# Performance work log

Measured on AMD Instinct MI355X. Metric: run time of the kernel, lower is better.

## Reference

```python
import jax, jax.numpy as jnp
import numpy as np

T = 4096   # total packed tokens
NQ = 16    # query heads
NK = 4     # kv heads (GQA)
HN = 128   # head dim


def setup_inputs() -> dict:
    key = jax.random.key(0)
    kq, kk, kv = jax.random.split(key, 3)
    return {
        "query": jax.random.normal(kq, (T, NQ, HN), dtype=jnp.float32),
        "key": jax.random.normal(kk, (T, NK, HN), dtype=jnp.float32),
        "value": jax.random.normal(kv, (T, NK, HN), dtype=jnp.float32),
        # packed varlen boundaries (4 sequences)
        "cu_seqlens": jnp.array([0, 1536, 2048, 3584, 4096], dtype=jnp.int32),
    }


def reference(query, key, value, cu_seqlens):
    t, nq, hn = query.shape
    nk = key.shape[1]
    rep = nq // nk  # GQA expansion factor
    scale = hn ** -0.5
    # [h, t, d] layout (matches torch unsqueeze(0).permute(0,2,1,3), batch=1)
    q = jnp.transpose(query, (1, 0, 2))
    k = jnp.repeat(jnp.transpose(key, (1, 0, 2)), rep, axis=0)
    v = jnp.repeat(jnp.transpose(value, (1, 0, 2)), rep, axis=0)
    # full scores [h, t, t]
    scores = jnp.einsum('hqd,hkd->hqk', q, k) * scale
    # block-diagonal causal mask from cu_seqlens
    idx = jnp.arange(t)
    seg = jnp.searchsorted(cu_seqlens[1:], idx, side='right')  # segment id per token
    allowed = (seg[:, None] == seg[None, :]) & (idx[None, :] <= idx[:, None])
    scores = jnp.where(allowed[None, :, :], scores, -jnp.inf)
    p = jax.nn.softmax(scores, axis=-1)  # every row keeps its diagonal -> no NaN
    out = jnp.einsum('hqk,hkd->hqd', p, v)
    # [t, nq*hn]
    return jnp.transpose(out, (1, 0, 2)).reshape(t, nq * hn)
```

## Files before the change

### kernel.cpp

```cpp
#include <hip/hip_runtime.h>
#include <hip/hip_bf16.h>
#include <cstdint>
#include <cstddef>

#define NQH 16
#define NKH 4
#define HN 128
#define QBLK 64
#define KBLK 32
#define QSCALE 0.12751589542585458f

typedef __bf16 bf16x8 __attribute__((ext_vector_type(8)));
typedef float f32x4 __attribute__((ext_vector_type(4)));

__device__ __forceinline__ void gload16(const void* g, void* l) {
  __builtin_amdgcn_global_load_lds(
      (const __attribute__((address_space(1))) void*)g,
      (__attribute__((address_space(3))) void*)l, 16, 0, 0);
}

__global__ __launch_bounds__(256) void cvt_kv(const float* __restrict__ K,
                                              const float* __restrict__ V,
                                              __bf16* __restrict__ Kb,
                                              __bf16* __restrict__ Vb, int T) {
  const int nkblk = T * NKH * HN / 8 / 256;
  const int bid = blockIdx.x;
  if (bid < nkblk) {
    const size_t idx8 = ((size_t)bid * 256 + threadIdx.x) * 8;
    const int d = (int)(idx8 & 127);
    const int kvh = (int)((idx8 >> 7) & 3);
    const size_t t = idx8 >> 9;
    float4 a = *(const float4*)&K[idx8];
    float4 b = *(const float4*)&K[idx8 + 4];
    bf16x8 f;
    f[0] = (__bf16)a.x; f[1] = (__bf16)a.y; f[2] = (__bf16)a.z; f[3] = (__bf16)a.w;
    f[4] = (__bf16)b.x; f[5] = (__bf16)b.y; f[6] = (__bf16)b.z; f[7] = (__bf16)b.w;
    *(bf16x8*)&Kb[(size_t)kvh * T * HN + t * HN + d] = f;
  } else {
    const int ob = (bid - nkblk) * 2 + (threadIdx.x >> 7);
    const int bx = ob & (T / 8 - 1);
    const int kvh = ob / (T / 8);
    const int d = threadIdx.x & 127;
    const int t0 = bx * 8;
    bf16x8 f;
#pragma unroll
    for (int i = 0; i < 8; ++i)
      f[i] = (__bf16)V[(size_t)(t0 + i) * (NKH * HN) + kvh * HN + d];
    *(bf16x8*)&Vb[(size_t)kvh * HN * T + (size_t)d * T + t0] = f;
  }
}

template <bool MASKED>
__device__ __forceinline__ void attn_iter(
    const char* Kc, const char* Vc, const bf16x8 qfA[4], const bf16x8 qfB[4],
    int ln, int hi, int vslot, int limA, float& lA, f32x4* accA,
    float& lB, f32x4* accB) {
  bf16x8 kf[2][4];
#pragma unroll
  for (int c = 0; c < 2; ++c)
#pragma unroll
    for (int kc = 0; kc < 4; ++kc)
      kf[c][kc] = *(const bf16x8*)(Kc + (c * 16 + ln) * 256 +
                                   (((kc * 4 + hi) ^ (ln & 7)) << 4));

  f32x4 sA[2], sB[2];
#pragma unroll
  for (int c = 0; c < 2; ++c) {
    sA[c] = (f32x4){0.f, 0.f, 0.f, 0.f};
    sB[c] = (f32x4){0.f, 0.f, 0.f, 0.f};
  }
  __builtin_amdgcn_s_setprio(1);
#pragma unroll
  for (int kc = 0; kc < 4; ++kc) {
#pragma unroll
    for (int c = 0; c < 2; ++c) {
      sA[c] = __builtin_amdgcn_mfma_f32_16x16x32_bf16(kf[c][kc], qfA[kc], sA[c], 0, 0, 0);
      sB[c] = __builtin_amdgcn_mfma_f32_16x16x32_bf16(kf[c][kc], qfB[kc], sB[c], 0, 0, 0);
    }
  }
  __builtin_amdgcn_s_setprio(0);

  if (MASKED) {
    const int limB = limA + 16;
#pragma unroll
    for (int c = 0; c < 2; ++c)
#pragma unroll
      for (int i = 0; i < 4; ++i) {
        const int koff = hi * 8 + c * 4 + i;
        sA[c][i] = (koff <= limA) ? sA[c][i] : -1e30f;
        sB[c][i] = (koff <= limB) ? sB[c][i] : -1e30f;
      }
  }

  float pA[2][4], pB[2][4];
  float psA = 0.f, psB = 0.f;
#pragma unroll
  for (int c = 0; c < 2; ++c)
#pragma unroll
    for (int i = 0; i < 4; ++i) {
      pA[c][i] = exp2f(sA[c][i]); psA += pA[c][i];
      pB[c][i] = exp2f(sB[c][i]); psB += pB[c][i];
    }
  lA += psA; lB += psB;

  bf16x8 paA, paB;
#pragma unroll
  for (int e = 0; e < 8; ++e) {
    paA[e] = (__bf16)pA[e >> 2][e & 3];
    paB[e] = (__bf16)pB[e >> 2][e & 3];
  }

  __builtin_amdgcn_s_setprio(1);
#pragma unroll
  for (int dt = 0; dt < 8; ++dt) {
    const bf16x8 vb = *(const bf16x8*)(Vc + (dt * 16 + ln) * 64 + vslot);
    accA[dt] = __builtin_amdgcn_mfma_f32_16x16x32_bf16(vb, paA, accA[dt], 0, 0, 0);
    accB[dt] = __builtin_amdgcn_mfma_f32_16x16x32_bf16(vb, paB, accB[dt], 0, 0, 0);
  }
  __builtin_amdgcn_s_setprio(0);
}

__global__ __launch_bounds__(256, 2) void attn_jobs(
    const float* __restrict__ Q, const __bf16* __restrict__ Kb,
    const __bf16* __restrict__ Vb, const int* __restrict__ cu,
    float* __restrict__ O, int T, int nseg) {
  const int tid = threadIdx.x;
  const int w = tid >> 6, lane = tid & 63;
  const int g = w >> 1, wv = w & 1;
  const int ln = lane & 15, hi = lane >> 4;
  const int b = blockIdx.x;

  __shared__ __align__(16) char smem[66304];
  float* l1s = (float*)(smem + 65536);
  int* s_r2t = (int*)(smem + 65792);

  if (w == 0) {
    const int t2 = lane;
    const int r0t = t2 << 6;
    int st = 0;
    for (int s = 1; s < nseg; ++s) { const int c = cu[s]; if (c <= r0t) st = c; }
    const int dep = r0t + QBLK - st;
    int rk = 0;
    for (int j = 0; j < 64; ++j) {
      const int dj = __shfl(dep, j);
      rk += (dj > dep) || (dj == dep && j < t2);
    }
    s_r2t[rk] = t2;
  }
  __syncthreads();

  const int gl = wv * 64 + lane;
  const int Rb = gl >> 4, sK = gl & 15;
  int key_j[4];
#pragma unroll
  for (int j = 0; j < 4; ++j)
    key_j[j] = ((Rb >> 2) << 3) + (Rb & 3) + ((j & 1) << 4) + ((j >> 1) << 2);
  const int kcolE = (sK ^ Rb) << 3;
  const int d = gl >> 2, sV = gl & 3;
  const int swz_d = (d & 3) ^ ((d >> 2) & 3);
  const int vkeyE = (sV ^ swz_d) << 3;
  const int vslot = ((hi ^ (ln & 3) ^ ((ln >> 2) & 3)) << 4);
  const int relA = wv * 32 + ln;

#pragma unroll 1
  for (int job = 0; job < 2; ++job) {
    if (job) __syncthreads();
    const int rank = job ? (1023 - b) : b;
    const int h = rank & 15;
    const int kvh = h >> 2;
    const int r0 = s_r2t[rank >> 4] << 6;

    int st0 = 0;
    for (int s = 1; s < nseg; ++s) { const int c = cu[s]; if (c <= r0) st0 = c; }
    const int kstart = st0;
    const int n0 = (r0 + QBLK - kstart) >> 6;
    const int gbeg = kstart + g * n0 * KBLK;

    const __bf16* KbH = Kb + (size_t)kvh * T * HN;
    const __bf16* VbH = Vb + (size_t)kvh * HN * T;

    bf16x8 qfA[4], qfB[4];
    {
      const float* qpA = &Q[(size_t)(r0 + wv * 32 + ln) * (NQH * HN) + h * HN];
      const float* qpB = qpA + (size_t)16 * (NQH * HN);
#pragma unroll
      for (int kc = 0; kc < 4; ++kc) {
        float4 a0 = *(const float4*)(qpA + kc * 32 + hi * 8);
        float4 a1 = *(const float4*)(qpA + kc * 32 + hi * 8 + 4);
        float4 b0 = *(const float4*)(qpB + kc * 32 + hi * 8);
        float4 b1 = *(const float4*)(qpB + kc * 32 + hi * 8 + 4);
        bf16x8 fa, fb;
        fa[0] = (__bf16)(a0.x * QSCALE); fa[1] = (__bf16)(a0.y * QSCALE);
        fa[2] = (__bf16)(a0.z * QSCALE); fa[3] = (__bf16)(a0.w * QSCALE);
        fa[4] = (__bf16)(a1.x * QSCALE); fa[5] = (__bf16)(a1.y * QSCALE);
        fa[6] = (__bf16)(a1.z * QSCALE); fa[7] = (__bf16)(a1.w * QSCALE);
        fb[0] = (__bf16)(b0.x * QSCALE); fb[1] = (__bf16)(b0.y * QSCALE);
        fb[2] = (__bf16)(b0.z * QSCALE); fb[3] = (__bf16)(b0.w * QSCALE);
        fb[4] = (__bf16)(b1.x * QSCALE); fb[5] = (__bf16)(b1.y * QSCALE);
        fb[6] = (__bf16)(b1.z * QSCALE); fb[7] = (__bf16)(b1.w * QSCALE);
        qfA[kc] = fa; qfB[kc] = fb;
      }
    }

    float lA = 0.f, lB = 0.f;
    f32x4 accA[8], accB[8];
#pragma unroll
    for (int dt = 0; dt < 8; ++dt) {
      accA[dt] = (f32x4){0.f, 0.f, 0.f, 0.f};
      accB[dt] = (f32x4){0.f, 0.f, 0.f, 0.f};
    }

#define ISSUE_TILE(buf, kb_)                                                   \
  {                                                                            \
    char* base_ = smem + (((g << 1) | (buf)) << 14);                           \
    char* lK_ = base_ + gl * 16;                                               \
    char* lV_ = base_ + 8192 + gl * 16;                                        \
    _Pragma("unroll")                                                          \
    for (int j = 0; j < 4; ++j)                                                \
      gload16(KbH + (size_t)((kb_) + key_j[j]) * HN + kcolE, lK_ + j * 2048);  \
    _Pragma("unroll")                                                          \
    for (int j = 0; j < 4; ++j)                                                \
      gload16(VbH + (size_t)(d + 32 * j) * T + (kb_) + vkeyE, lV_ + j * 2048); \
  }

    ISSUE_TILE(0, gbeg);
    if (n0 > 1) ISSUE_TILE(1, gbeg + KBLK);

    for (int it = 0; it < n0; ++it) {
      const int cur = it & 1;
      if (it < n0 - 1) {
        asm volatile("s_waitcnt vmcnt(8)" ::: "memory");
      } else {
        asm volatile("s_waitcnt vmcnt(0)" ::: "memory");
      }
      __builtin_amdgcn_sched_barrier(0);
      __builtin_amdgcn_s_barrier();
      const char* tb = smem + (((g << 1) | cur) << 14);
      const int kb = gbeg + it * KBLK;
      if (kb >= r0)
        attn_iter<true>(tb, tb + 8192, qfA, qfB, ln, hi, vslot,
                        relA - (kb - r0), lA, accA, lB, accB);
      else
        attn_iter<false>(tb, tb + 8192, qfA, qfB, ln, hi, vslot, 0, lA, accA,
                         lB, accB);
      asm volatile("s_waitcnt lgkmcnt(0)" ::: "memory");
      __builtin_amdgcn_sched_barrier(0);
      __builtin_amdgcn_s_barrier();
      if (it + 2 < n0) ISSUE_TILE(cur, kb + 2 * KBLK);
    }
#undef ISSUE_TILE

    lA += __shfl_xor(lA, 16); lA += __shfl_xor(lA, 32);
    lB += __shfl_xor(lB, 16); lB += __shfl_xor(lB, 32);

    __syncthreads();

    float* accf = (float*)smem;
    if (g == 1) {
      if (hi == 0) {
        l1s[relA] = lA;
        l1s[relA + 16] = lB;
      }
#pragma unroll
      for (int dt = 0; dt < 8; ++dt) {
        *(f32x4*)&accf[relA * 128 + ((dt ^ (relA & 7)) << 4) + (hi << 2)] = accA[dt];
        *(f32x4*)&accf[(relA + 16) * 128 + ((dt ^ ((relA + 16) & 7)) << 4) + (hi << 2)] = accB[dt];
      }
    }
    __syncthreads();
    if (g == 0) {
#pragma unroll
      for (int set = 0; set < 2; ++set) {
        const int row = relA + set * 16;
        const float lg = set ? lB : lA;
        f32x4* acc = set ? accB : accA;
        const float inv = 1.0f / (lg + l1s[row]);
        float* op = &O[(size_t)(r0 + row) * (NQH * HN) + h * HN];
#pragma unroll
        for (int dt = 0; dt < 8; ++dt) {
          const f32x4 a1 = *(const f32x4*)&accf[row * 128 + ((dt ^ (row & 7)) << 4) + (hi << 2)];
          const f32x4 res = (acc[dt] + a1) * inv;
          *(f32x4*)&op[dt * 16 + hi * 4] = res;
        }
      }
    }
  }
}

extern "C" void kernel_launch(void* const* d_in, const int* in_sizes, int n_in,
                              void* d_out, int out_size, void* d_ws, size_t ws_size,
                              hipStream_t stream) {
  const float* Q = (const float*)d_in[0];
  const float* K = (const float*)d_in[1];
  const float* V = (const float*)d_in[2];
  const int* cu = (const int*)d_in[3];
  float* O = (float*)d_out;

  const int T = in_sizes[0] / (NQH * HN);
  const int nseg = in_sizes[3] - 1;

  const size_t need = (size_t)2 * NKH * T * HN * sizeof(__bf16);
  if (ws_size < need) return;

  __bf16* Kb = (__bf16*)d_ws;
  __bf16* Vb = (__bf16*)d_ws + (size_t)NKH * T * HN;

  const int nkblk = T * NKH * HN / 8 / 256;
  cvt_kv<<<2 * nkblk, 256, 0, stream>>>(K, V, Kb, Vb, T);

  attn_jobs<<<512, 256, 0, stream>>>(Q, Kb, Vb, cu, O, T, nseg);
}
```

Measured before the change: 61.06 us.

## Software-pipeline QK of next tile with softmax-PV of previous tile

Splits each attention iteration into a QK phase and a softmax+PV phase, then runs tile i's QK MFMAs alongside the exp/PV work of tile i-1. This lets the exp/convert VALU work overlap matrix-core work. V gets a triple-buffered LDS ring so the previous tile's V stays live, which raises LDS use to 80KB per block and adds registers for the carried scores. The tile-rank lookup also moves from an LDS table to a ballot and shuffle, dropping one __syncthreads. The cost is higher register and LDS pressure, which may limit the two-blocks-per-CU occupancy target.

```diff
diff --git a/kernel.cpp b/kernel.cpp
--- a/kernel.cpp
+++ b/kernel.cpp
@@ -9,6 +9,7 @@
 #define QBLK 64
 #define KBLK 32
 #define QSCALE 0.12751589542585458f
+#define GRP_B 40960
 
 typedef __bf16 bf16x8 __attribute__((ext_vector_type(8)));
 typedef float f32x4 __attribute__((ext_vector_type(4)));
@@ -50,11 +51,9 @@
   }
 }
 
-template <bool MASKED>
-__device__ __forceinline__ void attn_iter(
-    const char* Kc, const char* Vc, const bf16x8 qfA[4], const bf16x8 qfB[4],
-    int ln, int hi, int vslot, int limA, float& lA, f32x4* accA,
-    float& lB, f32x4* accB) {
+__device__ __forceinline__ void qk_phase(const char* Kc, const bf16x8 qfA[4],
+                                         const bf16x8 qfB[4], int ln, int hi,
+                                         f32x4 sA[2], f32x4 sB[2]) {
   bf16x8 kf[2][4];
 #pragma unroll
   for (int c = 0; c < 2; ++c)
@@ -62,14 +61,11 @@
     for (int kc = 0; kc < 4; ++kc)
       kf[c][kc] = *(const bf16x8*)(Kc + (c * 16 + ln) * 256 +
                                    (((kc * 4 + hi) ^ (ln & 7)) << 4));
-
-  f32x4 sA[2], sB[2];
 #pragma unroll
   for (int c = 0; c < 2; ++c) {
     sA[c] = (f32x4){0.f, 0.f, 0.f, 0.f};
     sB[c] = (f32x4){0.f, 0.f, 0.f, 0.f};
   }
-  __builtin_amdgcn_s_setprio(1);
 #pragma unroll
   for (int kc = 0; kc < 4; ++kc) {
 #pragma unroll
@@ -78,28 +74,27 @@
       sB[c] = __builtin_amdgcn_mfma_f32_16x16x32_bf16(kf[c][kc], qfB[kc], sB[c], 0, 0, 0);
     }
   }
-  __builtin_amdgcn_s_setprio(0);
-
-  if (MASKED) {
-    const int limB = limA + 16;
-#pragma unroll
-    for (int c = 0; c < 2; ++c)
-#pragma unroll
-      for (int i = 0; i < 4; ++i) {
-        const int koff = hi * 8 + c * 4 + i;
-        sA[c][i] = (koff <= limA) ? sA[c][i] : -1e30f;
-        sB[c][i] = (koff <= limB) ? sB[c][i] : -1e30f;
-      }
-  }
-
+}
+
+template <bool MASKED>
+__device__ __forceinline__ void smpv_phase(const char* Vc, const f32x4 sA[2],
+                                           const f32x4 sB[2], int ln, int hi,
+                                           int vslot, int limA, float& lA,
+                                           f32x4* accA, float& lB, f32x4* accB) {
   float pA[2][4], pB[2][4];
   float psA = 0.f, psB = 0.f;
 #pragma unroll
   for (int c = 0; c < 2; ++c)
 #pragma unroll
     for (int i = 0; i < 4; ++i) {
-      pA[c][i] = exp2f(sA[c][i]); psA += pA[c][i];
-      pB[c][i] = exp2f(sB[c][i]); psB += pB[c][i];
+      float va = sA[c][i], vb2 = sB[c][i];
+      if (MASKED) {
+        const int koff = hi * 8 + c * 4 + i;
+        va = (koff <= limA) ? va : -1e30f;
+        vb2 = (koff <= limA + 16) ? vb2 : -1e30f;
+      }
+      pA[c][i] = exp2f(va); psA += pA[c][i];
+      pB[c][i] = exp2f(vb2); psB += pB[c][i];
     }
   lA += psA; lB += psB;
 
@@ -109,18 +104,15 @@
     paA[e] = (__bf16)pA[e >> 2][e & 3];
     paB[e] = (__bf16)pB[e >> 2][e & 3];
   }
-
-  __builtin_amdgcn_s_setprio(1);
 #pragma unroll
   for (int dt = 0; dt < 8; ++dt) {
     const bf16x8 vb = *(const bf16x8*)(Vc + (dt * 16 + ln) * 64 + vslot);
     accA[dt] = __builtin_amdgcn_mfma_f32_16x16x32_bf16(vb, paA, accA[dt], 0, 0, 0);
     accB[dt] = __builtin_amdgcn_mfma_f32_16x16x32_bf16(vb, paB, accB[dt], 0, 0, 0);
   }
-  __builtin_amdgcn_s_setprio(0);
-}
-
-__global__ __launch_bounds__(256, 2) void attn_jobs(
+}
+
+__global__ __launch_bounds__(256, 2) void attn_pl(
     const float* __restrict__ Q, const __bf16* __restrict__ Kb,
     const __bf16* __restrict__ Vb, const int* __restrict__ cu,
     float* __restrict__ O, int T, int nseg) {
@@ -130,24 +122,20 @@
   const int ln = lane & 15, hi = lane >> 4;
   const int b = blockIdx.x;
 
-  __shared__ __align__(16) char smem[66304];
-  float* l1s = (float*)(smem + 65536);
-  int* s_r2t = (int*)(smem + 65792);
-
-  if (w == 0) {
-    const int t2 = lane;
-    const int r0t = t2 << 6;
-    int st = 0;
-    for (int s = 1; s < nseg; ++s) { const int c = cu[s]; if (c <= r0t) st = c; }
-    const int dep = r0t + QBLK - st;
-    int rk = 0;
-    for (int j = 0; j < 64; ++j) {
-      const int dj = __shfl(dep, j);
-      rk += (dj > dep) || (dj == dep && j < t2);
-    }
-    s_r2t[rk] = t2;
-  }
-  __syncthreads();
+  __shared__ __align__(16) char smem[81920];
+  float* l1s = (float*)(smem + 32768);
+
+  int st_l = 0;
+  {
+    const int r0t = lane << 6;
+    for (int s = 1; s < nseg; ++s) { const int c = cu[s]; if (c <= r0t) st_l = c; }
+  }
+  const int dep = (lane << 6) + QBLK - st_l;
+  int rk = 0;
+  for (int j = 0; j < 64; ++j) {
+    const int dj = __shfl(dep, j);
+    rk += (dj > dep) || (dj == dep && j < lane);
+  }
 
   const int gl = wv * 64 + lane;
   const int Rb = gl >> 4, sK = gl & 15;
@@ -168,11 +156,10 @@
     const int rank = job ? (1023 - b) : b;
     const int h = rank & 15;
     const int kvh = h >> 2;
-    const int r0 = s_r2t[rank >> 4] << 6;
-
-    int st0 = 0;
-    for (int s = 1; s < nseg; ++s) { const int c = cu[s]; if (c <= r0) st0 = c; }
-    const int kstart = st0;
+    const unsigned long long msk = __ballot(rk == (rank >> 4));
+    const int tile = (int)__builtin_ctzll(msk);
+    const int r0 = tile << 6;
+    const int kstart = __shfl(st_l, tile);
     const int n0 = (r0 + QBLK - kstart) >> 6;
     const int gbeg = kstart + g * n0 * KBLK;
 
@@ -210,11 +197,12 @@
       accB[dt] = (f32x4){0.f, 0.f, 0.f, 0.f};
     }
 
-#define ISSUE_TILE(buf, kb_)                                                   \
+    char* grp = smem + g * GRP_B;
+
+#define ISSUE_TILE(kb_, ks_, vs_)                                              \
   {                                                                            \
-    char* base_ = smem + (((g << 1) | (buf)) << 14);                           \
-    char* lK_ = base_ + gl * 16;                                               \
-    char* lV_ = base_ + 8192 + gl * 16;                                        \
+    char* lK_ = grp + (ks_) * 8192 + gl * 16;                                  \
+    char* lV_ = grp + 16384 + (vs_) * 8192 + gl * 16;                          \
     _Pragma("unroll")                                                          \
     for (int j = 0; j < 4; ++j)                                                \
       gload16(KbH + (size_t)((kb_) + key_j[j]) * HN + kcolE, lK_ + j * 2048);  \
@@ -223,11 +211,14 @@
       gload16(VbH + (size_t)(d + 32 * j) * T + (kb_) + vkeyE, lV_ + j * 2048); \
   }
 
-    ISSUE_TILE(0, gbeg);
-    if (n0 > 1) ISSUE_TILE(1, gbeg + KBLK);
+    ISSUE_TILE(gbeg, 0, 0);
+    if (n0 > 1) ISSUE_TILE(gbeg + KBLK, 1, 1);
+
+    f32x4 sAp[2], sBp[2];
+    int kbp = 0;
+    int vsl = 0;
 
     for (int it = 0; it < n0; ++it) {
-      const int cur = it & 1;
       if (it < n0 - 1) {
         asm volatile("s_waitcnt vmcnt(8)" ::: "memory");
       } else {
@@ -235,20 +226,43 @@
       }
       __builtin_amdgcn_sched_barrier(0);
       __builtin_amdgcn_s_barrier();
-      const char* tb = smem + (((g << 1) | cur) << 14);
       const int kb = gbeg + it * KBLK;
-      if (kb >= r0)
-        attn_iter<true>(tb, tb + 8192, qfA, qfB, ln, hi, vslot,
-                        relA - (kb - r0), lA, accA, lB, accB);
-      else
-        attn_iter<false>(tb, tb + 8192, qfA, qfB, ln, hi, vslot, 0, lA, accA,
-                         lB, accB);
+      const int vold = (vsl == 0) ? 2 : vsl - 1;
+      const char* Kc = grp + (it & 1) * 8192;
+
+      __builtin_amdgcn_s_setprio(1);
+      f32x4 sA[2], sB[2];
+      qk_phase(Kc, qfA, qfB, ln, hi, sA, sB);
+      if (it > 0) {
+        const char* Vp = grp + 16384 + vold * 8192;
+        if (kbp >= r0)
+          smpv_phase<true>(Vp, sAp, sBp, ln, hi, vslot, relA - (kbp - r0), lA,
+                           accA, lB, accB);
+        else
+          smpv_phase<false>(Vp, sAp, sBp, ln, hi, vslot, 0, lA, accA, lB, accB);
+      }
+      __builtin_amdgcn_s_setprio(0);
+      sAp[0] = sA[0]; sAp[1] = sA[1];
+      sBp[0] = sB[0]; sBp[1] = sB[1];
+      kbp = kb;
+
       asm volatile("s_waitcnt lgkmcnt(0)" ::: "memory");
       __builtin_amdgcn_sched_barrier(0);
       __builtin_amdgcn_s_barrier();
-      if (it + 2 < n0) ISSUE_TILE(cur, kb + 2 * KBLK);
+      if (it + 2 < n0) ISSUE_TILE(kb + 2 * KBLK, it & 1, vold);
+      vsl = (vsl == 2) ? 0 : vsl + 1;
     }
 #undef ISSUE_TILE
+
+    {
+      const int vold = (vsl == 0) ? 2 : vsl - 1;
+      const char* Vp = grp + 16384 + vold * 8192;
+      if (kbp >= r0)
+        smpv_phase<true>(Vp, sAp, sBp, ln, hi, vslot, relA - (kbp - r0), lA,
+                         accA, lB, accB);
+      else
+        smpv_phase<false>(Vp, sAp, sBp, ln, hi, vslot, 0, lA, accA, lB, accB);
+    }
 
     lA += __shfl_xor(lA, 16); lA += __shfl_xor(lA, 32);
     lB += __shfl_xor(lB, 16); lB += __shfl_xor(lB, 32);
@@ -308,5 +322,5 @@
   const int nkblk = T * NKH * HN / 8 / 256;
   cvt_kv<<<2 * nkblk, 256, 0, stream>>>(K, V, Kb, Vb, T);
 
-  attn_jobs<<<512, 256, 0, stream>>>(Q, Kb, Vb, cu, O, T, nseg);
-}
+  attn_pl<<<512, 256, 0, stream>>>(Q, Kb, Vb, cu, O, T, nseg);
+}
```

After: 61.04 us. About the same (-0.0%).
